# Optimization experiments

Hardware: AMD Instinct MI355X
Metric: run time of the kernel (lower is better)

Reference implementation:

```python
import jax, jax.numpy as jnp
import numpy as np

B, C, H, W = 16, 256, 64, 64


def _conv1x1(x, w, b):
    # x: [B,C,H,W], w: [O,C], b: [O]
    return jnp.einsum('oc,bchw->bohw', w, x) + b[None, :, None, None]


def _maxpool2(x):
    b, c, h, w = x.shape
    return x.reshape(b, c, h // 2, 2, w // 2, 2).max(axis=(3, 5))


def setup_inputs() -> dict:
    key = jax.random.key(0)
    ks = jax.random.split(key, 10)
    c8, c2 = C // 8, C // 2
    s = lambda fan_in: 1.0 / np.sqrt(fan_in)
    return {
        'x': jax.random.normal(ks[0], (B, C, H, W), dtype=jnp.float32),
        'query_w': jax.random.normal(ks[1], (c8, C), dtype=jnp.float32) * s(C),
        'query_b': jnp.zeros((c8,), dtype=jnp.float32),
        'key_w': jax.random.normal(ks[2], (c8, C), dtype=jnp.float32) * s(C),
        'key_b': jnp.zeros((c8,), dtype=jnp.float32),
        'val_w': jax.random.normal(ks[3], (c2, C), dtype=jnp.float32) * s(C),
        'val_b': jnp.zeros((c2,), dtype=jnp.float32),
        'val2_w': jax.random.normal(ks[4], (C, c2), dtype=jnp.float32) * s(c2),
        'val2_b': jnp.zeros((C,), dtype=jnp.float32),
        'gamma': jnp.zeros((1,), dtype=jnp.float32) + 0.5,  # nonzero so attention path contributes
    }


def reference(x, query_w, query_b, key_w, key_b, val_w, val_b, val2_w, val2_b, gamma):
    b, nc, h, w = x.shape
    loc = h * w
    down = loc // 4
    c8, c2 = nc // 8, nc // 2

    # query: conv then raw view to [B, HW, C//8] (NOT a permute; faithful to torch .view)
    q = _conv1x1(x, query_w, query_b)              # [B, C/8, H, W]
    q = q.reshape(b, loc, c8)                      # raw reshape, mixes channel/spatial

    # key: conv -> 2x2 maxpool -> raw view -> permute(0,2,1)
    k = _maxpool2(_conv1x1(x, key_w, key_b))       # [B, C/8, H/2, W/2]
    k = k.reshape(b, down, c8).transpose(0, 2, 1)  # [B, C/8, down]

    # value: conv -> 2x2 maxpool -> raw view
    v = _maxpool2(_conv1x1(x, val_w, val_b))       # [B, C/2, H/2, W/2]
    v = v.reshape(b, down, c2)                     # [B, down, C/2]

    attn = jnp.einsum('bqd,bdk->bqk', q, k)        # [B, HW, down], no 1/sqrt(d)
    attn_weights = jax.nn.softmax(attn, axis=1)    # softmax over QUERY axis (dim=1), as in source
    applied = jnp.einsum('bqk,bkc->bqc', attn_weights, v)  # [B, HW, C/2]

    # raw view back to [B, C/2, w, h] (note w,h swapped in source)
    applied = applied.reshape(b, c2, w, h)
    out = _conv1x1(applied, val2_w, val2_b)        # [B, C, w, h]
    return gamma * out + x
```

## Files before the change

kernel.cpp:

```cpp
#include <hip/hip_runtime.h>
#include <hip/hip_bf16.h>


typedef short s8v __attribute__((ext_vector_type(8)));
typedef float f4v __attribute__((ext_vector_type(4)));
typedef unsigned short u16v8 __attribute__((ext_vector_type(8)));

#define MFMA16(a, b, c) __builtin_amdgcn_mfma_f32_16x16x32_bf16((a), (b), (c), 0, 0, 0)
#define LOG2E 1.4426950408889634f

__device__ __forceinline__ unsigned short f2b(float f) {
    __hip_bfloat16 h = __float2bfloat16(f);
    return *reinterpret_cast<unsigned short*>(&h);
}
__device__ __forceinline__ float b2f(unsigned short u) {
    union { unsigned int i; float f; } v; v.i = ((unsigned int)u) << 16; return v.f;
}

__global__ __launch_bounds__(256) void prologue(const float* __restrict__ x,
                                                unsigned short* __restrict__ xbt,
                                                const float* __restrict__ qw, const float* __restrict__ qb,
                                                const float* __restrict__ kw, const float* __restrict__ kb,
                                                const float* __restrict__ vw, const float* __restrict__ vb,
                                                const float* __restrict__ v2w,
                                                unsigned short* __restrict__ wqkv,
                                                float* __restrict__ bias,
                                                unsigned short* __restrict__ w2b) {
    int bid = blockIdx.x;
    if (bid < 4096) {
        __shared__ float tile[64][65];
        int bx = bid & 3, by = (bid >> 2) & 63, bz = bid >> 8;
        size_t base = (size_t)bz * 1048576;
        int r0 = bx * 64, c0 = by * 64;
        int rl = threadIdx.x >> 3;
        int g  = threadIdx.x & 7;
        #pragma unroll
        for (int rr = 0; rr < 2; ++rr) {
            int r = rr * 32 + rl;
            const float* p = x + base + (size_t)(r0 + r) * 4096 + c0 + g * 8;
            float4 a = *(const float4*)p;
            float4 bq = *(const float4*)(p + 4);
            tile[r][g * 8 + 0] = a.x;  tile[r][g * 8 + 1] = a.y;
            tile[r][g * 8 + 2] = a.z;  tile[r][g * 8 + 3] = a.w;
            tile[r][g * 8 + 4] = bq.x; tile[r][g * 8 + 5] = bq.y;
            tile[r][g * 8 + 6] = bq.z; tile[r][g * 8 + 7] = bq.w;
        }
        __syncthreads();
        #pragma unroll
        for (int rr = 0; rr < 2; ++rr) {
            int c = rr * 32 + rl;
            u16v8 o;
            #pragma unroll
            for (int i = 0; i < 8; ++i) o[i] = f2b(tile[g * 8 + i][c]);
            *(u16v8*)(xbt + base + (size_t)(c0 + c) * 256 + r0 + g * 8) = o;
        }
    } else {
        int i = (bid - 4096) * 256 + threadIdx.x;
        if (i < 49152) {
            int r = i >> 8, c = i & 255; float v;
            if (r < 32)       v = qw[r * 256 + c];
            else if (r < 64)  v = kw[(r - 32) * 256 + c] * LOG2E;
            else              v = vw[(r - 64) * 256 + c];
            wqkv[i] = f2b(v);
        } else if (i < 49152 + 32768) {
            int k = i - 49152; w2b[k] = f2b(v2w[k]);
        } else if (i < 49152 + 32768 + 192) {
            int r = i - 49152 - 32768;
            bias[r] = (r < 32) ? qb[r] : (r < 64 ? kb[r - 32] * LOG2E : vb[r - 64]);
        }
    }
}

__global__ __launch_bounds__(256) void transpose_scale_v(const unsigned short* __restrict__ src,
                                                         const float* __restrict__ rs,
                                                         unsigned short* __restrict__ dst) {
    __shared__ float tile[64][65];
    int b = blockIdx.z;
    size_t base = (size_t)b * 131072;
    int r0 = blockIdx.x * 64, c0 = blockIdx.y * 64;
    int tr = threadIdx.x >> 6, tc = threadIdx.x & 63;
    float scale = rs[b * 1024 + r0 + tc];
    for (int i = 0; i < 16; ++i) {
        int rl = i * 4 + tr;
        tile[rl][tc] = b2f(src[base + (size_t)(r0 + rl) * 128 + c0 + tc]);
    }
    __syncthreads();
    for (int i = 0; i < 16; ++i) {
        int cl = i * 4 + tr;
        int c = c0 + cl;
        int j = r0 + tc;
        int jc = j >> 7, jl = j & 127, g = jl >> 3, e = jl & 7;
        dst[base + jc * 16384 + c * 128 + ((g ^ (c & 7)) << 3) + e] =
            f2b(tile[tc][cl] * scale);
    }
}

__global__ __launch_bounds__(256) void qkv_pool(const unsigned short* __restrict__ wqkv,
                                                const float* __restrict__ bias,
                                                const unsigned short* __restrict__ xbt,
                                                unsigned short* __restrict__ qf,
                                                unsigned short* __restrict__ kf,
                                                unsigned short* __restrict__ vf) {
    int b = blockIdx.y, r = blockIdx.x;
    int p0 = r * 128;
    int wave = threadIdx.x >> 6, lane = threadIdx.x & 63;
    int m = lane & 15, quad = lane >> 4;
    const unsigned short* xb = xbt + (size_t)b * 4096 * 256;

    f4v acc[3][8] = {};
    for (int ks = 0; ks < 8; ++ks) {
        int k0 = ks * 32 + quad * 8;
        s8v afr[3];
        for (int mt = 0; mt < 3; ++mt)
            afr[mt] = *(const s8v*)(wqkv + (wave * 48 + mt * 16 + m) * 256 + k0);
        for (int nt = 0; nt < 8; ++nt) {
            s8v bfr = *(const s8v*)(xb + (size_t)(p0 + nt * 16 + m) * 256 + k0);
            for (int mt = 0; mt < 3; ++mt)
                acc[mt][nt] = MFMA16(afr[mt], bfr, acc[mt][nt]);
        }
    }
    for (int mt = 0; mt < 3; ++mt) {
        int obase = wave * 48 + mt * 16;
        if (obase < 32) {
            for (int reg = 0; reg < 4; ++reg) {
                int o = obase + quad * 4 + reg;
                float bi = bias[o];
                for (int nt = 0; nt < 8; ++nt)
                    qf[(size_t)b * 131072 + (size_t)o * 4096 + p0 + nt * 16 + m] =
                        f2b(acc[mt][nt][reg] + bi);
            }
        } else {
            for (int reg = 0; reg < 4; ++reg) {
                int o = obase + quad * 4 + reg;
                float bi = bias[o];
                for (int nt = 0; nt < 4; ++nt) {
                    float vv = fmaxf(acc[mt][nt][reg], acc[mt][nt + 4][reg]);
                    float ov = __shfl_xor(vv, 1);
                    if ((m & 1) == 0) {
                        float res = fmaxf(vv, ov) + bi;
                        int w2 = nt * 8 + (m >> 1);
                        int sp = r * 32 + w2;
                        if (o < 64) kf[(size_t)b * 32768 + (size_t)(o - 32) * 1024 + sp] = f2b(res);
                        else        vf[(size_t)b * 131072 + (size_t)(o - 64) * 1024 + sp] = f2b(res);
                    }
                }
            }
        }
    }
}

__global__ __launch_bounds__(256) void col_stats(const unsigned short* __restrict__ qf,
                                                 const unsigned short* __restrict__ kf,
                                                 float* __restrict__ rs) {
    __shared__ float red[4][16];
    int b = blockIdx.y, j0 = blockIdx.x * 16;
    int wave = threadIdx.x >> 6, lane = threadIdx.x & 63;
    int m = lane & 15, quad = lane >> 4;
    const unsigned short* qb = qf + (size_t)b * 131072;
    f4v zero = {0.f, 0.f, 0.f, 0.f};

    s8v kfr = *(const s8v*)(kf + (size_t)b * 32768 + (size_t)(j0 + m) * 32 + quad * 8);

    float sm = 0.f;
    for (int it = wave; it < 256; it += 4) {
        s8v afr = *(const s8v*)(qb + (size_t)(it * 16 + m) * 32 + quad * 8);
        f4v s = MFMA16(afr, kfr, zero);
        sm += (exp2f(s[0]) + exp2f(s[1])) + (exp2f(s[2]) + exp2f(s[3]));
    }
    sm += __shfl_xor(sm, 16);
    sm += __shfl_xor(sm, 32);
    if (lane < 16) red[wave][m] = sm;
    __syncthreads();
    if (threadIdx.x < 16) {
        float S = (red[0][threadIdx.x] + red[1][threadIdx.x]) +
                  (red[2][threadIdx.x] + red[3][threadIdx.x]);
        rs[b * 1024 + j0 + threadIdx.x] = 1.0f / S;
    }
}

__global__ __launch_bounds__(512, 4) void attn_fused(const unsigned short* __restrict__ qf,
                                                     const unsigned short* __restrict__ kf,
                                                     const unsigned short* __restrict__ vsw,
                                                     unsigned short* __restrict__ fa) {
    __shared__ alignas(16) unsigned short VS[16384];
    __shared__ alignas(16) unsigned short PT[16384];
    int b = blockIdx.y, l0 = blockIdx.x * 128;
    int tid = threadIdx.x;
    int wave = tid >> 6, lane = tid & 63;
    int m = lane & 15, quad = lane >> 4;
    int ls = wave * 16;
    const unsigned short* qb = qf + (size_t)b * 131072;
    const unsigned short* kb = kf + (size_t)b * 32768;
    const unsigned short* vb = vsw + (size_t)b * 131072;

    s8v qa = *(const s8v*)(qb + (size_t)(l0 + ls + m) * 32 + quad * 8);
    f4v acc[8] = {};
    f4v zero = {0.f, 0.f, 0.f, 0.f};

    for (int jc = 0; jc < 8; ++jc) {
        const unsigned short* src = vb + jc * 16384 + tid * 8;
        u16v8 t0 = *(const u16v8*)(src);
        u16v8 t1 = *(const u16v8*)(src + 4096);
        u16v8 t2 = *(const u16v8*)(src + 8192);
        u16v8 t3 = *(const u16v8*)(src + 12288);

        int j0 = jc * 128;
        int l = ls + m;
        for (int jt = 0; jt < 8; ++jt) {
            s8v kfr = *(const s8v*)(kb + (size_t)(j0 + jt * 16 + m) * 32 + quad * 8);
            f4v st = MFMA16(kfr, qa, zero);
            unsigned int u0 = ((unsigned)f2b(exp2f(st[1])) << 16) |
                              (unsigned)f2b(exp2f(st[0]));
            unsigned int u1 = ((unsigned)f2b(exp2f(st[3])) << 16) |
                              (unsigned)f2b(exp2f(st[2]));
            int g = jt * 2 + (quad >> 1);
            int sub = (quad & 1) * 4;
            uint2 uu; uu.x = u0; uu.y = u1;
            *(uint2*)(&PT[l * 128 + ((g ^ (l & 7)) << 3) + sub]) = uu;
        }

        __syncthreads();

        {
            unsigned short* dstl = VS + tid * 8;
            *(u16v8*)(dstl)         = t0;
            *(u16v8*)(dstl + 4096)  = t1;
            *(u16v8*)(dstl + 8192)  = t2;
            *(u16v8*)(dstl + 12288) = t3;
        }

        __syncthreads();

        __builtin_amdgcn_s_setprio(1);
        for (int ks = 0; ks < 4; ++ks) {
            int gp = ks * 4 + quad;
            s8v pa = *(const s8v*)(&PT[l * 128 + ((gp ^ (l & 7)) << 3)]);
            for (int ct = 0; ct < 8; ++ct) {
                int c = ct * 16 + m;
                s8v vfr = *(const s8v*)(&VS[c * 128 + ((gp ^ (c & 7)) << 3)]);
                acc[ct] = MFMA16(pa, vfr, acc[ct]);
            }
        }
        __builtin_amdgcn_s_setprio(0);
    }
    for (int ct = 0; ct < 8; ++ct)
        for (int reg = 0; reg < 4; ++reg) {
            int l = l0 + ls + quad * 4 + reg;
            fa[(size_t)b * 524288 + (size_t)l * 128 + ct * 16 + m] = f2b(acc[ct][reg]);
        }
}

__global__ __launch_bounds__(256, 4) void final_gemm(const unsigned short* __restrict__ w2b,
                                                     const float* __restrict__ v2b,
                                                     const float* __restrict__ gamma,
                                                     const unsigned short* __restrict__ fa,
                                                     const float* __restrict__ x,
                                                     float* __restrict__ out) {
    __shared__ alignas(16) unsigned short gt[64][136];
    int b = blockIdx.z, bx = blockIdx.x;
    int p0 = bx * 64;
    int page = bx >> 1;
    int c0 = (bx & 1) * 64;
    int wave = threadIdx.x >> 6, lane = threadIdx.x & 63;
    int m = lane & 15, quad = lane >> 4;
    int obase = blockIdx.y * 128 + wave * 32;

    int row  = threadIdx.x >> 1;
    int half = threadIdx.x & 1;
    const unsigned short* fr = fa + (size_t)b * 524288 +
                               (size_t)(row * 32 + page) * 128 + c0 + half * 32;
    u16v8 t0 = *(const u16v8*)(fr);
    u16v8 t1 = *(const u16v8*)(fr + 8);
    u16v8 t2 = *(const u16v8*)(fr + 16);
    u16v8 t3 = *(const u16v8*)(fr + 24);

    float4 xv[2][4];
    #pragma unroll
    for (int mt = 0; mt < 2; ++mt) {
        size_t xrow = (size_t)b * 1048576 + (size_t)(obase + mt * 16 + m) * 4096;
        #pragma unroll
        for (int nt = 0; nt < 4; ++nt)
            xv[mt][nt] = *(const float4*)(x + xrow + p0 + nt * 16 + quad * 4);
    }

    {
        int pb = half * 32;
        #pragma unroll
        for (int i = 0; i < 8; ++i) {
            gt[pb + i][row]      = t0[i];
            gt[pb + 8 + i][row]  = t1[i];
            gt[pb + 16 + i][row] = t2[i];
            gt[pb + 24 + i][row] = t3[i];
        }
    }
    __syncthreads();

    f4v acc[2][4] = {};
    for (int ks = 0; ks < 4; ++ks) {
        int k0 = ks * 32 + quad * 8;
        s8v afr[2], bfr[4];
        #pragma unroll
        for (int mt = 0; mt < 2; ++mt)
            afr[mt] = *(const s8v*)(w2b + (obase + mt * 16 + m) * 128 + k0);
        #pragma unroll
        for (int nt = 0; nt < 4; ++nt)
            bfr[nt] = *(const s8v*)(&gt[nt * 16 + m][k0]);
        #pragma unroll
        for (int mt = 0; mt < 2; ++mt)
            #pragma unroll
            for (int nt = 0; nt < 4; ++nt)
                acc[mt][nt] = MFMA16(bfr[nt], afr[mt], acc[mt][nt]);
    }
    float g = gamma[0];
    #pragma unroll
    for (int mt = 0; mt < 2; ++mt) {
        int o = obase + mt * 16 + m;
        float bi = v2b[o];
        size_t xrow = (size_t)b * 1048576 + (size_t)o * 4096;
        #pragma unroll
        for (int nt = 0; nt < 4; ++nt) {
            size_t xi = xrow + p0 + nt * 16 + quad * 4;
            float4 ov;
            ov.x = g * (acc[mt][nt][0] + bi) + xv[mt][nt].x;
            ov.y = g * (acc[mt][nt][1] + bi) + xv[mt][nt].y;
            ov.z = g * (acc[mt][nt][2] + bi) + xv[mt][nt].z;
            ov.w = g * (acc[mt][nt][3] + bi) + xv[mt][nt].w;
            *(float4*)(out + xi) = ov;
        }
    }
}

extern "C" void kernel_launch(void* const* d_in, const int* in_sizes, int n_in,
                              void* d_out, int out_size, void* d_ws, size_t ws_size,
                              hipStream_t stream) {
    const float* x    = (const float*)d_in[0];
    const float* qw   = (const float*)d_in[1];
    const float* qb   = (const float*)d_in[2];
    const float* kw   = (const float*)d_in[3];
    const float* kb   = (const float*)d_in[4];
    const float* vw   = (const float*)d_in[5];
    const float* vb   = (const float*)d_in[6];
    const float* v2w  = (const float*)d_in[7];
    const float* v2b  = (const float*)d_in[8];
    const float* gamma = (const float*)d_in[9];
    float* out = (float*)d_out;

    char* ws = (char*)d_ws;
    size_t off = 0;
    auto alloc = [&](size_t bytes) { size_t o = off; off = (off + bytes + 255) & ~(size_t)255; return o; };
    unsigned short* wqkv = (unsigned short*)(ws + alloc(192 * 256 * 2));
    unsigned short* w2b  = (unsigned short*)(ws + alloc(256 * 128 * 2));
    float*          bias = (float*)(ws + alloc(192 * 4));
    float*          rs   = (float*)(ws + alloc((size_t)16 * 1024 * 4));
    unsigned short* qf   = (unsigned short*)(ws + alloc((size_t)16 * 131072 * 2));
    unsigned short* kf   = (unsigned short*)(ws + alloc((size_t)16 * 32768 * 2));
    unsigned short* vf   = (unsigned short*)(ws + alloc((size_t)16 * 131072 * 2));
    unsigned short* vt   = (unsigned short*)(ws + alloc((size_t)16 * 131072 * 2));
    unsigned short* fa   = (unsigned short*)(ws + alloc((size_t)16 * 524288 * 2));
    unsigned short* xbt  = (unsigned short*)(ws + alloc((size_t)16 * 4096 * 256 * 2));
    (void)ws_size; (void)in_sizes; (void)n_in; (void)out_size;

    prologue<<<4417, 256, 0, stream>>>(x, xbt, qw, qb, kw, kb, vw, vb, v2w, wqkv, bias, w2b);
    qkv_pool<<<dim3(32, 16), 256, 0, stream>>>(wqkv, bias, xbt, qf, kf, vf);
    col_stats<<<dim3(64, 16), 256, 0, stream>>>(qf, kf, rs);
    transpose_scale_v<<<dim3(16, 2, 16), 256, 0, stream>>>(vf, rs, vt);
    attn_fused<<<dim3(32, 16), 512, 0, stream>>>(qf, kf, vt, fa);
    final_gemm<<<dim3(64, 2, 16), 256, 0, stream>>>(w2b, v2b, gamma, fa, x, out);
}
```

Baseline: 247.9 us.

## Fuse x transpose/bf16 cast into qkv_pool via LDS; widen col_stats tiles

Drops the separate prologue pass that transposed all of x into a bf16 workspace buffer. Each qkv_pool block now loads its 128-pixel slab of fp32 x directly, converts it to bf16 and stores it transposed in a swizzled 64KB LDS tile, then runs the MFMAs from LDS. This removes a full write and re-read of a 32MB intermediate. The trade is that the 64KB of LDS per block may limit occupancy. Separately, col_stats now handles 32 key columns per block with two MFMAs per Q fragment, halving the grid and Q reloads.

Result: faster. 228.6 us (-7.8%).

```diff
diff --git a/kernel.cpp b/kernel.cpp
--- a/kernel.cpp
+++ b/kernel.cpp
@@ -5,6 +5,7 @@
 typedef short s8v __attribute__((ext_vector_type(8)));
 typedef float f4v __attribute__((ext_vector_type(4)));
 typedef unsigned short u16v8 __attribute__((ext_vector_type(8)));
+typedef unsigned short u16v4 __attribute__((ext_vector_type(4)));
 
 #define MFMA16(a, b, c) __builtin_amdgcn_mfma_f32_16x16x32_bf16((a), (b), (c), 0, 0, 0)
 #define LOG2E 1.4426950408889634f
@@ -17,95 +18,65 @@
     union { unsigned int i; float f; } v; v.i = ((unsigned int)u) << 16; return v.f;
 }
 
-__global__ __launch_bounds__(256) void prologue(const float* __restrict__ x,
-                                                unsigned short* __restrict__ xbt,
-                                                const float* __restrict__ qw, const float* __restrict__ qb,
-                                                const float* __restrict__ kw, const float* __restrict__ kb,
-                                                const float* __restrict__ vw, const float* __restrict__ vb,
-                                                const float* __restrict__ v2w,
-                                                unsigned short* __restrict__ wqkv,
-                                                float* __restrict__ bias,
-                                                unsigned short* __restrict__ w2b) {
-    int bid = blockIdx.x;
-    if (bid < 4096) {
-        __shared__ float tile[64][65];
-        int bx = bid & 3, by = (bid >> 2) & 63, bz = bid >> 8;
-        size_t base = (size_t)bz * 1048576;
-        int r0 = bx * 64, c0 = by * 64;
-        int rl = threadIdx.x >> 3;
-        int g  = threadIdx.x & 7;
-        #pragma unroll
-        for (int rr = 0; rr < 2; ++rr) {
-            int r = rr * 32 + rl;
-            const float* p = x + base + (size_t)(r0 + r) * 4096 + c0 + g * 8;
-            float4 a = *(const float4*)p;
-            float4 bq = *(const float4*)(p + 4);
-            tile[r][g * 8 + 0] = a.x;  tile[r][g * 8 + 1] = a.y;
-            tile[r][g * 8 + 2] = a.z;  tile[r][g * 8 + 3] = a.w;
-            tile[r][g * 8 + 4] = bq.x; tile[r][g * 8 + 5] = bq.y;
-            tile[r][g * 8 + 6] = bq.z; tile[r][g * 8 + 7] = bq.w;
-        }
-        __syncthreads();
-        #pragma unroll
-        for (int rr = 0; rr < 2; ++rr) {
-            int c = rr * 32 + rl;
-            u16v8 o;
-            #pragma unroll
-            for (int i = 0; i < 8; ++i) o[i] = f2b(tile[g * 8 + i][c]);
-            *(u16v8*)(xbt + base + (size_t)(c0 + c) * 256 + r0 + g * 8) = o;
-        }
-    } else {
-        int i = (bid - 4096) * 256 + threadIdx.x;
-        if (i < 49152) {
-            int r = i >> 8, c = i & 255; float v;
-            if (r < 32)       v = qw[r * 256 + c];
-            else if (r < 64)  v = kw[(r - 32) * 256 + c] * LOG2E;
-            else              v = vw[(r - 64) * 256 + c];
-            wqkv[i] = f2b(v);
-        } else if (i < 49152 + 32768) {
-            int k = i - 49152; w2b[k] = f2b(v2w[k]);
-        } else if (i < 49152 + 32768 + 192) {
-            int r = i - 49152 - 32768;
-            bias[r] = (r < 32) ? qb[r] : (r < 64 ? kb[r - 32] * LOG2E : vb[r - 64]);
-        }
-    }
-}
-
-__global__ __launch_bounds__(256) void transpose_scale_v(const unsigned short* __restrict__ src,
-                                                         const float* __restrict__ rs,
-                                                         unsigned short* __restrict__ dst) {
-    __shared__ float tile[64][65];
-    int b = blockIdx.z;
-    size_t base = (size_t)b * 131072;
-    int r0 = blockIdx.x * 64, c0 = blockIdx.y * 64;
-    int tr = threadIdx.x >> 6, tc = threadIdx.x & 63;
-    float scale = rs[b * 1024 + r0 + tc];
-    for (int i = 0; i < 16; ++i) {
-        int rl = i * 4 + tr;
-        tile[rl][tc] = b2f(src[base + (size_t)(r0 + rl) * 128 + c0 + tc]);
-    }
-    __syncthreads();
-    for (int i = 0; i < 16; ++i) {
-        int cl = i * 4 + tr;
-        int c = c0 + cl;
-        int j = r0 + tc;
-        int jc = j >> 7, jl = j & 127, g = jl >> 3, e = jl & 7;
-        dst[base + jc * 16384 + c * 128 + ((g ^ (c & 7)) << 3) + e] =
-            f2b(tile[tc][cl] * scale);
+__global__ void prep_weights(const float* __restrict__ qw, const float* __restrict__ qb,
+                             const float* __restrict__ kw, const float* __restrict__ kb,
+                             const float* __restrict__ vw, const float* __restrict__ vb,
+                             const float* __restrict__ v2w,
+                             unsigned short* __restrict__ wqkv, float* __restrict__ bias,
+                             unsigned short* __restrict__ w2b) {
+    int i = blockIdx.x * 256 + threadIdx.x;
+    if (i < 49152) {
+        int r = i >> 8, c = i & 255; float v;
+        if (r < 32)       v = qw[r * 256 + c];
+        else if (r < 64)  v = kw[(r - 32) * 256 + c] * LOG2E;
+        else              v = vw[(r - 64) * 256 + c];
+        wqkv[i] = f2b(v);
+    } else if (i < 49152 + 32768) {
+        int k = i - 49152; w2b[k] = f2b(v2w[k]);
+    } else if (i < 49152 + 32768 + 192) {
+        int r = i - 49152 - 32768;
+        bias[r] = (r < 32) ? qb[r] : (r < 64 ? kb[r - 32] * LOG2E : vb[r - 64]);
     }
 }
 
 __global__ __launch_bounds__(256) void qkv_pool(const unsigned short* __restrict__ wqkv,
                                                 const float* __restrict__ bias,
-                                                const unsigned short* __restrict__ xbt,
+                                                const float* __restrict__ x,
                                                 unsigned short* __restrict__ qf,
                                                 unsigned short* __restrict__ kf,
                                                 unsigned short* __restrict__ vf) {
+    __shared__ alignas(16) unsigned short xt[32768];
     int b = blockIdx.y, r = blockIdx.x;
     int p0 = r * 128;
-    int wave = threadIdx.x >> 6, lane = threadIdx.x & 63;
+    int t = threadIdx.x;
+    int wave = t >> 6, lane = t & 63;
     int m = lane & 15, quad = lane >> 4;
-    const unsigned short* xb = xbt + (size_t)b * 4096 * 256;
+    const float* xb = x + (size_t)b * 1048576;
+
+    {
+        int pq = t & 31, kb = t >> 5;
+        #pragma unroll
+        for (int s = 0; s < 8; ++s) {
+            int kbase = s * 32 + kb * 4;
+            float4 f0 = *(const float4*)(xb + (size_t)(kbase + 0) * 4096 + p0 + pq * 4);
+            float4 f1 = *(const float4*)(xb + (size_t)(kbase + 1) * 4096 + p0 + pq * 4);
+            float4 f2 = *(const float4*)(xb + (size_t)(kbase + 2) * 4096 + p0 + pq * 4);
+            float4 f3 = *(const float4*)(xb + (size_t)(kbase + 3) * 4096 + p0 + pq * 4);
+            int ko = kbase >> 3, sub = kbase & 7;
+            #pragma unroll
+            for (int pi = 0; pi < 4; ++pi) {
+                int p = pq * 4 + pi;
+                float a0 = pi == 0 ? f0.x : pi == 1 ? f0.y : pi == 2 ? f0.z : f0.w;
+                float a1 = pi == 0 ? f1.x : pi == 1 ? f1.y : pi == 2 ? f1.z : f1.w;
+                float a2 = pi == 0 ? f2.x : pi == 1 ? f2.y : pi == 2 ? f2.z : f2.w;
+                float a3 = pi == 0 ? f3.x : pi == 1 ? f3.y : pi == 2 ? f3.z : f3.w;
+                u16v4 pk; pk[0] = f2b(a0); pk[1] = f2b(a1); pk[2] = f2b(a2); pk[3] = f2b(a3);
+                int swz = (p & 7) ^ ((p >> 2) & 7);
+                *(u16v4*)(&xt[p * 256 + ((ko ^ swz) << 3) + sub]) = pk;
+            }
+        }
+    }
+    __syncthreads();
 
     f4v acc[3][8] = {};
     for (int ks = 0; ks < 8; ++ks) {
@@ -114,7 +85,9 @@
         for (int mt = 0; mt < 3; ++mt)
             afr[mt] = *(const s8v*)(wqkv + (wave * 48 + mt * 16 + m) * 256 + k0);
         for (int nt = 0; nt < 8; ++nt) {
-            s8v bfr = *(const s8v*)(xb + (size_t)(p0 + nt * 16 + m) * 256 + k0);
+            int p = nt * 16 + m;
+            int swz = (p & 7) ^ ((p >> 2) & 7);
+            s8v bfr = *(const s8v*)(&xt[p * 256 + (((ks * 4 + quad) ^ swz) << 3)]);
             for (int mt = 0; mt < 3; ++mt)
                 acc[mt][nt] = MFMA16(afr[mt], bfr, acc[mt][nt]);
         }
@@ -152,29 +125,56 @@
 __global__ __launch_bounds__(256) void col_stats(const unsigned short* __restrict__ qf,
                                                  const unsigned short* __restrict__ kf,
                                                  float* __restrict__ rs) {
-    __shared__ float red[4][16];
-    int b = blockIdx.y, j0 = blockIdx.x * 16;
+    __shared__ float red[4][32];
+    int b = blockIdx.y, j0 = blockIdx.x * 32;
     int wave = threadIdx.x >> 6, lane = threadIdx.x & 63;
     int m = lane & 15, quad = lane >> 4;
     const unsigned short* qb = qf + (size_t)b * 131072;
     f4v zero = {0.f, 0.f, 0.f, 0.f};
 
-    s8v kfr = *(const s8v*)(kf + (size_t)b * 32768 + (size_t)(j0 + m) * 32 + quad * 8);
-
-    float sm = 0.f;
+    s8v kfr0 = *(const s8v*)(kf + (size_t)b * 32768 + (size_t)(j0 + m) * 32 + quad * 8);
+    s8v kfr1 = *(const s8v*)(kf + (size_t)b * 32768 + (size_t)(j0 + 16 + m) * 32 + quad * 8);
+
+    float sm0 = 0.f, sm1 = 0.f;
     for (int it = wave; it < 256; it += 4) {
         s8v afr = *(const s8v*)(qb + (size_t)(it * 16 + m) * 32 + quad * 8);
-        f4v s = MFMA16(afr, kfr, zero);
-        sm += (exp2f(s[0]) + exp2f(s[1])) + (exp2f(s[2]) + exp2f(s[3]));
-    }
-    sm += __shfl_xor(sm, 16);
-    sm += __shfl_xor(sm, 32);
-    if (lane < 16) red[wave][m] = sm;
+        f4v s0 = MFMA16(afr, kfr0, zero);
+        f4v s1 = MFMA16(afr, kfr1, zero);
+        sm0 += (exp2f(s0[0]) + exp2f(s0[1])) + (exp2f(s0[2]) + exp2f(s0[3]));
+        sm1 += (exp2f(s1[0]) + exp2f(s1[1])) + (exp2f(s1[2]) + exp2f(s1[3]));
+    }
+    sm0 += __shfl_xor(sm0, 16); sm0 += __shfl_xor(sm0, 32);
+    sm1 += __shfl_xor(sm1, 16); sm1 += __shfl_xor(sm1, 32);
+    if (lane < 16) { red[wave][m] = sm0; red[wave][16 + m] = sm1; }
     __syncthreads();
-    if (threadIdx.x < 16) {
+    if (threadIdx.x < 32) {
         float S = (red[0][threadIdx.x] + red[1][threadIdx.x]) +
                   (red[2][threadIdx.x] + red[3][threadIdx.x]);
         rs[b * 1024 + j0 + threadIdx.x] = 1.0f / S;
+    }
+}
+
+__global__ __launch_bounds__(256) void transpose_scale_v(const unsigned short* __restrict__ src,
+                                                         const float* __restrict__ rs,
+                                                         unsigned short* __restrict__ dst) {
+    __shared__ float tile[64][65];
+    int b = blockIdx.z;
+    size_t base = (size_t)b * 131072;
+    int r0 = blockIdx.x * 64, c0 = blockIdx.y * 64;
+    int tr = threadIdx.x >> 6, tc = threadIdx.x & 63;
+    float scale = rs[b * 1024 + r0 + tc];
+    for (int i = 0; i < 16; ++i) {
+        int rl = i * 4 + tr;
+        tile[rl][tc] = b2f(src[base + (size_t)(r0 + rl) * 128 + c0 + tc]);
+    }
+    __syncthreads();
+    for (int i = 0; i < 16; ++i) {
+        int cl = i * 4 + tr;
+        int c = c0 + cl;
+        int j = r0 + tc;
+        int jc = j >> 7, jl = j & 127, g = jl >> 3, e = jl & 7;
+        dst[base + jc * 16384 + c * 128 + ((g ^ (c & 7)) << 3) + e] =
+            f2b(tile[tc][cl] * scale);
     }
 }
 
@@ -357,12 +357,11 @@
     unsigned short* vf   = (unsigned short*)(ws + alloc((size_t)16 * 131072 * 2));
     unsigned short* vt   = (unsigned short*)(ws + alloc((size_t)16 * 131072 * 2));
     unsigned short* fa   = (unsigned short*)(ws + alloc((size_t)16 * 524288 * 2));
-    unsigned short* xbt  = (unsigned short*)(ws + alloc((size_t)16 * 4096 * 256 * 2));
     (void)ws_size; (void)in_sizes; (void)n_in; (void)out_size;
 
-    prologue<<<4417, 256, 0, stream>>>(x, xbt, qw, qb, kw, kb, vw, vb, v2w, wqkv, bias, w2b);
-    qkv_pool<<<dim3(32, 16), 256, 0, stream>>>(wqkv, bias, xbt, qf, kf, vf);
-    col_stats<<<dim3(64, 16), 256, 0, stream>>>(qf, kf, rs);
+    prep_weights<<<321, 256, 0, stream>>>(qw, qb, kw, kb, vw, vb, v2w, wqkv, bias, w2b);
+    qkv_pool<<<dim3(32, 16), 256, 0, stream>>>(wqkv, bias, x, qf, kf, vf);
+    col_stats<<<dim3(32, 16), 256, 0, stream>>>(qf, kf, rs);
     transpose_scale_v<<<dim3(16, 2, 16), 256, 0, stream>>>(vf, rs, vt);
     attn_fused<<<dim3(32, 16), 512, 0, stream>>>(qf, kf, vt, fa);
     final_gemm<<<dim3(64, 2, 16), 256, 0, stream>>>(w2b, v2b, gamma, fa, x, out);
```
